# Optimization experiments

Hardware: AMD Instinct MI355X
Metric: run time of the kernel (lower is better)

## Reference

```python
import jax, jax.numpy as jnp
import numpy as np

H, F, O, T = 2048, 2048, 2048, 4096  # hidden, feature, output, seq_len


def setup_inputs() -> dict:
    key = jax.random.key(0)
    kx, kf, ki, kc, ko, ky = jax.random.split(key, 6)
    xav = lambda k, shp: jax.random.uniform(k, shp, jnp.float32, -1.0, 1.0) * np.sqrt(6.0 / (shp[0] + shp[1]))
    return {
        "X": jax.random.normal(kx, (T, F), jnp.float32),
        "wf": xav(kf, (H, H + F)), "bf": jnp.zeros((H,), jnp.float32),
        "wi": xav(ki, (H, H + F)), "bi": jnp.zeros((H,), jnp.float32),
        "wc": xav(kc, (H, H + F)), "bc": jnp.zeros((H,), jnp.float32),
        "wo": xav(ko, (H, H + F)), "bo": jnp.zeros((H,), jnp.float32),
        "wy": xav(ky, (O, H)), "by": jnp.zeros((O,), jnp.float32),
    }


def reference(X, wf, bf, wi, bi, wc, bc, wo, bo, wy, by):
    h = wf.shape[0]
    # Fuse the four gate GEMVs into one (same math as four separate matmuls).
    W4 = jnp.concatenate([wf, wi, wc, wo], axis=0)   # (4H, H+F)
    b4 = jnp.concatenate([bf, bi, bc, bo], axis=0)   # (4H,)

    def step(carry, x_t):
        hs, cs = carry
        z = W4 @ jnp.concatenate([hs, x_t]) + b4      # (4H,)
        f = jax.nn.sigmoid(z[:h])
        i = jax.nn.sigmoid(z[h:2 * h])
        g = jnp.tanh(z[2 * h:3 * h])
        o = jax.nn.sigmoid(z[3 * h:])
        cs = f * cs + i * g
        hs = o * jnp.tanh(cs)
        return (hs, cs), None

    init = (jnp.zeros((h,), X.dtype), jnp.zeros((h,), X.dtype))
    (h_T, _), _ = jax.lax.scan(step, init, X)
    # Original returns only the final timestep's projection.
    return wy @ h_T + by
```

## Files before the change

### kernel.cpp

```cpp
#include <hip/hip_runtime.h>
#include <hip/hip_fp16.h>

typedef _Float16 h8 __attribute__((ext_vector_type(8)));
typedef _Float16 h2 __attribute__((ext_vector_type(2)));
typedef float    f4 __attribute__((ext_vector_type(4)));
typedef unsigned int u32;
typedef u32 u32x4 __attribute__((ext_vector_type(4)));

#define HDIM 2048
#define FDIM 2048
#define TSEQ 4096
#define NR   8192

__device__ __forceinline__ float sigmoidf_(float x) { return 1.0f / (1.0f + __expf(-x)); }
__device__ __forceinline__ float tanhf_(float x)    { return 1.0f - 2.0f / (1.0f + __expf(2.0f * x)); }

__device__ __forceinline__ int swz(int g) { return (g & ~15) | ((g ^ (g >> 4)) & 15); }

__global__ __launch_bounds__(256) void gemm_zx(
    const float* __restrict__ X,
    const float* __restrict__ wfp, const float* __restrict__ wip,
    const float* __restrict__ wcp, const float* __restrict__ wop,
    _Float16* __restrict__ Zx)
{
    __shared__ __align__(16) _Float16 As[128 * 32];
    __shared__ __align__(16) _Float16 Bs[128 * 32];
    const int tid  = threadIdx.x;
    const int lane = tid & 63;
    const int wv   = tid >> 6;
    const int bm   = blockIdx.x & 31;
    const int bn   = blockIdx.x >> 5;
    const int m0 = bm * 128, n0 = bn * 128;
    const int g = n0 >> 11;
    const float* wsrc = (g == 0) ? wfp : (g == 1) ? wip : (g == 2) ? wcp : wop;
    const int nr0 = n0 & 2047;

    f4 acc[4][4];
    #pragma unroll
    for (int i = 0; i < 4; ++i)
        #pragma unroll
        for (int j = 0; j < 4; ++j) acc[i][j] = (f4){0.f, 0.f, 0.f, 0.f};

    const int wm = (wv >> 1) * 64, wn = (wv & 1) * 64;
    const int fr = lane & 15, kg = lane >> 4;

    for (int k0 = 0; k0 < FDIM; k0 += 32) {
        __syncthreads();
        #pragma unroll
        for (int r = 0; r < 2; ++r) {
            const int row = r * 64 + (tid >> 2);
            const int col = (tid & 3) * 8;
            const float* ax = &X[(size_t)(m0 + row) * FDIM + k0 + col];
            f4 a0 = *(const f4*)ax, a1 = *(const f4*)(ax + 4);
            h8 av = { (_Float16)a0[0], (_Float16)a0[1], (_Float16)a0[2], (_Float16)a0[3],
                      (_Float16)a1[0], (_Float16)a1[1], (_Float16)a1[2], (_Float16)a1[3] };
            *(h8*)&As[row * 32 + col] = av;
            const float* bx = &wsrc[(size_t)(nr0 + row) * 4096 + 2048 + k0 + col];
            f4 b0 = *(const f4*)bx, b1 = *(const f4*)(bx + 4);
            h8 bv = { (_Float16)b0[0], (_Float16)b0[1], (_Float16)b0[2], (_Float16)b0[3],
                      (_Float16)b1[0], (_Float16)b1[1], (_Float16)b1[2], (_Float16)b1[3] };
            *(h8*)&Bs[row * 32 + col] = bv;
        }
        __syncthreads();
        h8 af[4], bf[4];
        #pragma unroll
        for (int i = 0; i < 4; ++i) af[i] = *(const h8*)&As[(wm + i * 16 + fr) * 32 + kg * 8];
        #pragma unroll
        for (int j = 0; j < 4; ++j) bf[j] = *(const h8*)&Bs[(wn + j * 16 + fr) * 32 + kg * 8];
        #pragma unroll
        for (int i = 0; i < 4; ++i)
            #pragma unroll
            for (int j = 0; j < 4; ++j)
                acc[i][j] = __builtin_amdgcn_mfma_f32_16x16x32_f16(af[i], bf[j], acc[i][j], 0, 0, 0);
    }
    #pragma unroll
    for (int i = 0; i < 4; ++i)
        #pragma unroll
        for (int j = 0; j < 4; ++j)
            #pragma unroll
            for (int q = 0; q < 4; ++q) {
                const int row = m0 + wm + i * 16 + (lane >> 4) * 4 + q;
                const int col = n0 + wn + j * 16 + (lane & 15);
                Zx[(size_t)row * NR + col] = (_Float16)acc[i][j][q];
            }
}

__global__ __launch_bounds__(256, 1) void lstm_rec(
    const float* __restrict__ wfp, const float* __restrict__ wip,
    const float* __restrict__ wcp, const float* __restrict__ wop,
    const float* __restrict__ bfv, const float* __restrict__ biv,
    const float* __restrict__ bcv, const float* __restrict__ bov,
    const _Float16* __restrict__ Zx,
    u32* __restrict__ hword,
    float* __restrict__ hfin)
{
    __shared__ __align__(16) u32 stage[HDIM];
    __shared__ float z_lds[32];
    __shared__ float c_lds[8];

    const int tid = threadIdx.x;
    const int w   = blockIdx.x;
    const int rg  = tid >> 5, cc = tid & 31;

    h8 wreg[4][8];
    #pragma unroll
    for (int q = 0; q < 4; ++q) {
        const int rl = rg * 4 + q;
        const int gg = rl >> 3, r8 = rl & 7;
        const float* src = ((gg == 0) ? wfp : (gg == 1) ? wip : (gg == 2) ? wcp : wop)
                           + (size_t)(8 * w + r8) * 4096 + cc * 64;
        #pragma unroll
        for (int i = 0; i < 8; ++i) {
            f4 a0 = *(const f4*)(src + i * 8);
            f4 a1 = *(const f4*)(src + i * 8 + 4);
            wreg[q][i] = (h8){ (_Float16)a0[0], (_Float16)a0[1], (_Float16)a0[2], (_Float16)a0[3],
                               (_Float16)a1[0], (_Float16)a1[1], (_Float16)a1[2], (_Float16)a1[3] };
        }
    }
    float bias0 = 0.f, bias1 = 0.f, bias2 = 0.f, bias3 = 0.f;
    if (tid < 8) {
        c_lds[tid] = 0.0f;
        bias0 = bfv[8 * w + tid]; bias1 = biv[8 * w + tid];
        bias2 = bcv[8 * w + tid]; bias3 = bov[8 * w + tid];
    }
    __syncthreads();

    #pragma unroll 1
    for (int t = 0; t < TSEQ; ++t) {
        float zx0 = 0.f, zx1 = 0.f, zx2 = 0.f, zx3 = 0.f;
        if (tid < 8) {
            const _Float16* zp = Zx + (size_t)t * NR + 8 * w + tid;
            zx0 = (float)zp[0]; zx1 = (float)zp[2048];
            zx2 = (float)zp[4096]; zx3 = (float)zp[6144];
        }

        const u32 texp = (u32)t << 16;
        const size_t slotbase = (size_t)(t & 1) * HDIM;

        if (tid < 64) {
            const u32* sp = hword + slotbase + (size_t)tid * 32;
            u32 s0, s1, s2, s3;
            for (;;) {
                asm volatile(
                    "global_load_dword %0, %4, off sc0 sc1\n\t"
                    "global_load_dword %1, %4, off offset:32 sc0 sc1\n\t"
                    "global_load_dword %2, %4, off offset:64 sc0 sc1\n\t"
                    "global_load_dword %3, %4, off offset:96 sc0 sc1\n\t"
                    "s_waitcnt vmcnt(0)"
                    : "=&v"(s0), "=&v"(s1), "=&v"(s2), "=&v"(s3)
                    : "v"(sp) : "memory");
                const u32 bad = ((s0 ^ texp) | (s1 ^ texp) | (s2 ^ texp) | (s3 ^ texp))
                                & 0xFFFF0000u;
                if (!bad) break;
                __builtin_amdgcn_s_sleep(2);
            }
        }
        __syncthreads();

        const u32* p = hword + slotbase + (size_t)tid * 8;
        u32x4 A, B;
        for (;;) {
            asm volatile(
                "global_load_dwordx4 %0, %2, off sc0 sc1\n\t"
                "global_load_dwordx4 %1, %2, off offset:16 sc0 sc1\n\t"
                "s_waitcnt vmcnt(0)"
                : "=&v"(A), "=&v"(B) : "v"(p) : "memory");
            const u32 bad = ((A.x ^ texp) | (A.y ^ texp) | (A.z ^ texp) | (A.w ^ texp) |
                             (B.x ^ texp) | (B.y ^ texp) | (B.z ^ texp) | (B.w ^ texp))
                            & 0xFFFF0000u;
            if (!bad) break;
            __builtin_amdgcn_s_sleep(1);
        }
        *(u32x4*)&stage[swz(tid * 2) * 4]     = A;
        *(u32x4*)&stage[swz(tid * 2 + 1) * 4] = B;
        __syncthreads();

        float acc[4] = {0.f, 0.f, 0.f, 0.f};
        #pragma unroll
        for (int i = 0; i < 8; ++i) {
            u32x4 ga = *(const u32x4*)&stage[swz(cc * 16 + 2 * i) * 4];
            u32x4 gb = *(const u32x4*)&stage[swz(cc * 16 + 2 * i + 1) * 4];
            const h2 h0  = __builtin_bit_cast(h2, (u32)((ga.x & 0xffffu) | (ga.y << 16)));
            const h2 h1  = __builtin_bit_cast(h2, (u32)((ga.z & 0xffffu) | (ga.w << 16)));
            const h2 h2v = __builtin_bit_cast(h2, (u32)((gb.x & 0xffffu) | (gb.y << 16)));
            const h2 h3  = __builtin_bit_cast(h2, (u32)((gb.z & 0xffffu) | (gb.w << 16)));
            #pragma unroll
            for (int q = 0; q < 4; ++q) {
                const h8 wv8 = wreg[q][i];
                acc[q] = __builtin_amdgcn_fdot2((h2){wv8[0], wv8[1]}, h0,  acc[q], false);
                acc[q] = __builtin_amdgcn_fdot2((h2){wv8[2], wv8[3]}, h1,  acc[q], false);
                acc[q] = __builtin_amdgcn_fdot2((h2){wv8[4], wv8[5]}, h2v, acc[q], false);
                acc[q] = __builtin_amdgcn_fdot2((h2){wv8[6], wv8[7]}, h3,  acc[q], false);
            }
        }
        #pragma unroll
        for (int m = 16; m >= 1; m >>= 1) {
            #pragma unroll
            for (int q = 0; q < 4; ++q) acc[q] += __shfl_xor(acc[q], m, 64);
        }
        if (cc == 0) {
            #pragma unroll
            for (int q = 0; q < 4; ++q) z_lds[rg * 4 + q] = acc[q];
        }
        __syncthreads();
        if (tid < 8) {
            const float zf = z_lds[tid]      + zx0 + bias0;
            const float zi = z_lds[8 + tid]  + zx1 + bias1;
            const float zc = z_lds[16 + tid] + zx2 + bias2;
            const float zo = z_lds[24 + tid] + zx3 + bias3;
            const float f  = sigmoidf_(zf);
            const float i_ = sigmoidf_(zi);
            const float g_ = tanhf_(zc);
            const float o  = sigmoidf_(zo);
            const float cn = f * c_lds[tid] + i_ * g_;
            c_lds[tid] = cn;
            const float hn = o * tanhf_(cn);
            const unsigned short hb =
                __builtin_bit_cast(unsigned short, (_Float16)hn);
            const u32 word = ((u32)(t + 1) << 16) | (u32)hb;
            u32* op = hword + (size_t)((t + 1) & 1) * HDIM + 8 * w + tid;
            asm volatile("global_store_dword %0, %1, off sc0 sc1"
                         :: "v"(op), "v"(word) : "memory");
            if (t == TSEQ - 1) hfin[8 * w + tid] = hn;
        }
    }
}

__global__ __launch_bounds__(256) void proj(
    const float* __restrict__ wy, const float* __restrict__ byv,
    const float* __restrict__ hfin, float* __restrict__ y)
{
    const int row = blockIdx.x;
    const float* wr = wy + (size_t)row * HDIM;
    float s = 0.f;
    for (int k = threadIdx.x * 4; k < HDIM; k += 256 * 4) {
        f4 wv = *(const f4*)&wr[k];
        f4 hv = *(const f4*)&hfin[k];
        s = fmaf(wv[0], hv[0], fmaf(wv[1], hv[1], fmaf(wv[2], hv[2], fmaf(wv[3], hv[3], s))));
    }
    #pragma unroll
    for (int m = 32; m >= 1; m >>= 1) s += __shfl_xor(s, m, 64);
    __shared__ float red[4];
    if ((threadIdx.x & 63) == 0) red[threadIdx.x >> 6] = s;
    __syncthreads();
    if (threadIdx.x == 0) y[row] = red[0] + red[1] + red[2] + red[3] + byv[row];
}

extern "C" void kernel_launch(void* const* d_in, const int* in_sizes, int n_in,
                              void* d_out, int out_size, void* d_ws, size_t ws_size,
                              hipStream_t stream)
{
    (void)in_sizes; (void)n_in; (void)out_size;
    const float* X   = (const float*)d_in[0];
    const float* wfp = (const float*)d_in[1];
    const float* bfv = (const float*)d_in[2];
    const float* wip = (const float*)d_in[3];
    const float* biv = (const float*)d_in[4];
    const float* wcp = (const float*)d_in[5];
    const float* bcv = (const float*)d_in[6];
    const float* wop = (const float*)d_in[7];
    const float* bov = (const float*)d_in[8];
    const float* wy  = (const float*)d_in[9];
    const float* byv = (const float*)d_in[10];
    float* y = (float*)d_out;

    char* ws = (char*)d_ws;
    const size_t need = ((size_t)64 << 20) + ((size_t)64 << 10);
    if (ws_size < need) return;

    _Float16* Zx  = (_Float16*)ws;
    u32* hword    = (u32*)(ws + ((size_t)64 << 20));
    float* hfin   = (float*)(ws + ((size_t)64 << 20) + (16 << 10));

    (void)hipMemsetAsync(hword, 0, 2 * HDIM * sizeof(u32), stream);
    gemm_zx<<<dim3(2048), dim3(256), 0, stream>>>(X, wfp, wip, wcp, wop, Zx);
    lstm_rec<<<dim3(256), dim3(256), 0, stream>>>(wfp, wip, wcp, wop,
                                                  bfv, biv, bcv, bov,
                                                  Zx, hword, hfin);
    proj<<<dim3(2048), dim3(256), 0, stream>>>(wy, byv, hfin, y);
}
```

Measured before the change: 9.978 ms.

## Map one hidden unit per row group to drop LDS gate exchange and barrier

Reassigns the weight rows so that each 32-lane row group holds the four gate rows (f, i, c, o) of a single hidden unit. After the shuffle reduction the group leader can then apply the nonlinearities and update the cell state held in a register, with no LDS staging and no __syncthreads on the per-step critical path. It also removes the sleep from the spin-wait poll and publishes h through an atomic swap rather than a plain store, aiming to cut latency in the cross-block handoff each step. In exchange, more threads perform the pointwise math, and tighter polling adds memory traffic.

```diff
diff --git a/kernel.cpp b/kernel.cpp
--- a/kernel.cpp
+++ b/kernel.cpp
@@ -95,8 +95,6 @@
     float* __restrict__ hfin)
 {
     __shared__ __align__(16) u32 stage[HDIM];
-    __shared__ float z_lds[32];
-    __shared__ float c_lds[8];
 
     const int tid = threadIdx.x;
     const int w   = blockIdx.x;
@@ -105,10 +103,8 @@
     h8 wreg[4][8];
     #pragma unroll
     for (int q = 0; q < 4; ++q) {
-        const int rl = rg * 4 + q;
-        const int gg = rl >> 3, r8 = rl & 7;
-        const float* src = ((gg == 0) ? wfp : (gg == 1) ? wip : (gg == 2) ? wcp : wop)
-                           + (size_t)(8 * w + r8) * 4096 + cc * 64;
+        const float* src = ((q == 0) ? wfp : (q == 1) ? wip : (q == 2) ? wcp : wop)
+                           + (size_t)(8 * w + rg) * 4096 + cc * 64;
         #pragma unroll
         for (int i = 0; i < 8; ++i) {
             f4 a0 = *(const f4*)(src + i * 8);
@@ -118,19 +114,19 @@
         }
     }
     float bias0 = 0.f, bias1 = 0.f, bias2 = 0.f, bias3 = 0.f;
-    if (tid < 8) {
-        c_lds[tid] = 0.0f;
-        bias0 = bfv[8 * w + tid]; bias1 = biv[8 * w + tid];
-        bias2 = bcv[8 * w + tid]; bias3 = bov[8 * w + tid];
-    }
-    __syncthreads();
+    float c_reg = 0.f;
+    if (cc == 0) {
+        bias0 = bfv[8 * w + rg]; bias1 = biv[8 * w + rg];
+        bias2 = bcv[8 * w + rg]; bias3 = bov[8 * w + rg];
+    }
+    const _Float16* zxp = Zx + 8 * w + rg;
 
     #pragma unroll 1
     for (int t = 0; t < TSEQ; ++t) {
         float zx0 = 0.f, zx1 = 0.f, zx2 = 0.f, zx3 = 0.f;
-        if (tid < 8) {
-            const _Float16* zp = Zx + (size_t)t * NR + 8 * w + tid;
-            zx0 = (float)zp[0]; zx1 = (float)zp[2048];
+        if (cc == 0) {
+            const _Float16* zp = zxp + (size_t)t * NR;
+            zx0 = (float)zp[0];    zx1 = (float)zp[2048];
             zx2 = (float)zp[4096]; zx3 = (float)zp[6144];
         }
 
@@ -152,7 +148,6 @@
                 const u32 bad = ((s0 ^ texp) | (s1 ^ texp) | (s2 ^ texp) | (s3 ^ texp))
                                 & 0xFFFF0000u;
                 if (!bad) break;
-                __builtin_amdgcn_s_sleep(2);
             }
         }
         __syncthreads();
@@ -198,30 +193,22 @@
             #pragma unroll
             for (int q = 0; q < 4; ++q) acc[q] += __shfl_xor(acc[q], m, 64);
         }
+
         if (cc == 0) {
-            #pragma unroll
-            for (int q = 0; q < 4; ++q) z_lds[rg * 4 + q] = acc[q];
-        }
-        __syncthreads();
-        if (tid < 8) {
-            const float zf = z_lds[tid]      + zx0 + bias0;
-            const float zi = z_lds[8 + tid]  + zx1 + bias1;
-            const float zc = z_lds[16 + tid] + zx2 + bias2;
-            const float zo = z_lds[24 + tid] + zx3 + bias3;
-            const float f  = sigmoidf_(zf);
-            const float i_ = sigmoidf_(zi);
-            const float g_ = tanhf_(zc);
-            const float o  = sigmoidf_(zo);
-            const float cn = f * c_lds[tid] + i_ * g_;
-            c_lds[tid] = cn;
+            const float f  = sigmoidf_(acc[0] + zx0 + bias0);
+            const float i_ = sigmoidf_(acc[1] + zx1 + bias1);
+            const float g_ = tanhf_(acc[2] + zx2 + bias2);
+            const float o  = sigmoidf_(acc[3] + zx3 + bias3);
+            const float cn = f * c_reg + i_ * g_;
+            c_reg = cn;
             const float hn = o * tanhf_(cn);
             const unsigned short hb =
                 __builtin_bit_cast(unsigned short, (_Float16)hn);
             const u32 word = ((u32)(t + 1) << 16) | (u32)hb;
-            u32* op = hword + (size_t)((t + 1) & 1) * HDIM + 8 * w + tid;
-            asm volatile("global_store_dword %0, %1, off sc0 sc1"
+            u32* op = hword + (size_t)((t + 1) & 1) * HDIM + 8 * w + rg;
+            asm volatile("global_atomic_swap %0, %1, off sc1"
                          :: "v"(op), "v"(word) : "memory");
-            if (t == TSEQ - 1) hfin[8 * w + tid] = hn;
+            if (t == TSEQ - 1) hfin[8 * w + rg] = hn;
         }
     }
 }
```

After: 10.04 ms. No clear change (+0.6%).
